# Performance work log

Hardware: AMD Instinct MI355X
Metric: run time of the kernel (lower is better)

## Reference

```python
import jax, jax.numpy as jnp
import numpy as np
import math

N, D = 4096, 1024


def setup_inputs() -> dict:
    key = jax.random.key(0)
    ks = jax.random.split(key, 8)
    vecs = jax.random.normal(ks[0], (N, D), dtype=jnp.float32)
    mass = jax.random.uniform(ks[1], (N,), dtype=jnp.float32)            # semantic mass in [0,1)
    hops = jax.random.uniform(ks[2], (N,), dtype=jnp.float32) * 5.0      # hop distances in [0,5)
    alive = jax.random.randint(ks[3], (N,), 0, 10) > 0
    is_photon = jax.random.randint(ks[4], (N,), 0, 10) == 0
    W_res_w = jax.random.normal(ks[5], (D, D), dtype=jnp.float32) / np.sqrt(D)
    W_res_b = jnp.zeros((D,), dtype=jnp.float32)
    w_conf_i = jax.random.normal(ks[6], (D,), dtype=jnp.float32) / np.sqrt(2 * D)
    w_conf_j = jax.random.normal(ks[7], (D,), dtype=jnp.float32) / np.sqrt(2 * D)
    b_conf = jnp.zeros((), dtype=jnp.float32)
    log_c = jnp.asarray(math.log(50.0), dtype=jnp.float32)  # 'relationship' domain
    log_G = jnp.zeros((), dtype=jnp.float32)
    return dict(vecs=vecs, mass=mass, hops=hops, alive=alive, is_photon=is_photon,
                W_res_w=W_res_w, W_res_b=W_res_b, w_conf_i=w_conf_i, w_conf_j=w_conf_j,
                b_conf=b_conf, log_c=log_c, log_G=log_G)


def reference(vecs, mass, hops, alive, is_photon, W_res_w, W_res_b,
              w_conf_i, w_conf_j, b_conf, log_c, log_G):
    n = vecs.shape[0]
    c = jnp.maximum(jnp.exp(log_c), 1e-6)
    G = jnp.exp(log_G)

    # Per-row quantities (phi() reads hops/photon from entity i).
    d_light = hops / c                                                   # [N]
    lam = jnp.where(is_photon, 1.0, jnp.exp(-d_light))                   # redshift, [N]
    r2 = jnp.maximum(d_light, 0.1) ** 2                                  # r_safe^2, [N]
    causal_decay = jnp.where(d_light <= 1.0, 1.0, jnp.exp(-d_light + 1.0))  # [N]

    # Causal mask: j must be strictly in the past (j < i).
    idx = jnp.arange(n)
    past = (idx[None, :] < idx[:, None]).astype(vecs.dtype)              # [N,N]
    C = past * causal_decay[:, None]

    # Gravity: G * m_i * m_j / r_i^2
    grav = G * (mass / r2)[:, None] * mass[None, :]                      # [N,N]

    # Resonance: cosine similarity of W_res projections (torch eps=1e-8 norm clamp).
    v = vecs @ W_res_w.T + W_res_b                                       # [N,D]
    vn = v / jnp.maximum(jnp.linalg.norm(v, axis=-1, keepdims=True), 1e-8)
    R = vn @ vn.T                                                        # [N,N]
    zero_norm = jnp.linalg.norm(vecs, axis=-1) < 1e-8                    # [N]
    R = jnp.where(zero_norm[:, None] | zero_norm[None, :], 0.0, R)

    # Conflict gate: sigmoid(W_conflict @ concat(v_i, v_j) + b) = sigmoid(s_i + s_j + b).
    s_i = vecs @ w_conf_i                                                # [N]
    s_j = vecs @ w_conf_j                                                # [N]
    conflict = jax.nn.sigmoid(s_i[:, None] + s_j[None, :] + b_conf)      # [N,N]

    phi_attract = lam[:, None] * grav * C * (0.5 + 0.5 * R)
    phi_repulse = -lam[:, None] * conflict * mass[:, None] * mass[None, :]
    phi = jnp.where(conflict > 0.8, phi_repulse, phi_attract)

    # Black holes and the diagonal produce zero field.
    gate = alive[:, None] & alive[None, :]
    phi = jnp.where(gate & (idx[:, None] != idx[None, :]), phi, 0.0)
    return phi
```

## Files before the change

kernel.cpp:

```cpp
#include <hip/hip_runtime.h>
#include <hip/hip_bf16.h>
#include <math.h>

#define NROW 4096
#define DIM  1024

typedef short v8s __attribute__((ext_vector_type(8)));
typedef float v4f __attribute__((ext_vector_type(4)));

#define GLD16(src, dst) __builtin_amdgcn_global_load_lds( \
    (const __attribute__((address_space(1))) void*)(src), \
    (__attribute__((address_space(3))) void*)(dst), 16, 0, 0)

__device__ __forceinline__ ushort f2bf(float f) {
    __hip_bfloat16 h = __float2bfloat16(f);
    union { __hip_bfloat16 h; ushort u; } x; x.h = h; return x.u;
}
__device__ __forceinline__ ushort4 cvt4(float4 a) {
    ushort4 r; r.x = f2bf(a.x); r.y = f2bf(a.y); r.z = f2bf(a.z); r.w = f2bf(a.w);
    return r;
}

__global__ __launch_bounds__(256) void k_stats(
    const float* vecs, const float* __restrict__ mass,
    const float* __restrict__ hops, const int* __restrict__ alive,
    const int* __restrict__ is_photon, const float* __restrict__ wci,
    const float* __restrict__ wcj, const float* __restrict__ logc,
    const float* __restrict__ logG, const float* __restrict__ bconf,
    const float* W,
    ushort* vsh, int vstr, ushort* wsh, int wstr,
    double* __restrict__ s_i, double* __restrict__ s_j,
    float* __restrict__ rowAtt, float* __restrict__ rowRep,
    float* __restrict__ massF, int* __restrict__ flags,
    float* __restrict__ rownorm)
{
    const int t = threadIdx.x;
    const int wid = t >> 6, lane = t & 63;

    if (blockIdx.x >= NROW / 4) {
        const int row = (blockIdx.x - NROW / 4) * 4 + wid;
        const float* wr = W + (size_t)row * DIM;
        ushort4 uc[4];
        #pragma unroll
        for (int q = 0; q < 4; ++q)
            uc[q] = cvt4(*(const float4*)&wr[lane * 4 + q * 256]);
        __syncthreads();
        ushort* wb = wsh + (size_t)row * wstr;
        #pragma unroll
        for (int q = 0; q < 4; ++q)
            *(ushort4*)&wb[lane * 4 + q * 256] = uc[q];
        return;
    }

    const int row = blockIdx.x * 4 + wid;
    const float* vr = vecs + (size_t)row * DIM;
    double di = 0.0, dj = 0.0, ss = 0.0;
    ushort4 uc[4];
    #pragma unroll
    for (int q = 0; q < 4; ++q) {
        int base = lane * 4 + q * 256;
        float4 pv = *(const float4*)&vr[base];
        float4 pi = *(const float4*)&wci[base];
        float4 pj = *(const float4*)&wcj[base];
        di += (double)pv.x * pi.x + (double)pv.y * pi.y + (double)pv.z * pi.z + (double)pv.w * pi.w;
        dj += (double)pv.x * pj.x + (double)pv.y * pj.y + (double)pv.z * pj.z + (double)pv.w * pj.w;
        ss += (double)pv.x * pv.x + (double)pv.y * pv.y + (double)pv.z * pv.z + (double)pv.w * pv.w;
        uc[q] = cvt4(pv);
    }
    __syncthreads();
    ushort* vb = vsh + (size_t)row * vstr;
    #pragma unroll
    for (int q = 0; q < 4; ++q)
        *(ushort4*)&vb[lane * 4 + q * 256] = uc[q];
    #pragma unroll
    for (int off = 32; off > 0; off >>= 1) {
        di += __shfl_down(di, off);
        dj += __shfl_down(dj, off);
        ss += __shfl_down(ss, off);
    }
    if (lane == 0) {
        double c  = fmax(exp((double)logc[0]), 1e-6);
        double G  = exp((double)logG[0]);
        double dl = (double)hops[row] / c;
        double lam = (is_photon[row] != 0) ? 1.0 : exp(-dl);
        double rs  = fmax(dl, 0.1);
        double cd  = (dl <= 1.0) ? 1.0 : exp(-dl + 1.0);
        double m   = (double)mass[row];
        s_i[row] = di;
        s_j[row] = dj + (double)bconf[0];
        rowAtt[row] = (float)(lam * G * m / (rs * rs) * cd);
        rowRep[row] = (float)(-lam * m);
        massF[row]  = (float)m;
        flags[row]  = ((alive[row] != 0) ? 1 : 0) | ((sqrt(ss) < 1e-8) ? 2 : 0);
        rownorm[row] = 0.0f;
    }
}

__global__ __launch_bounds__(256) void k_proj(
    const ushort* __restrict__ vsh, int vstr,
    const ushort* __restrict__ wsh, int wstr,
    const float* __restrict__ bias, ushort* __restrict__ vout,
    float* __restrict__ rownorm)
{
    __shared__ ushort As[64 * 64], Bs[64 * 64];
    const int t = threadIdx.x;
    const int m0 = blockIdx.y * 64, n0 = blockIdx.x * 64;
    const int wid = t >> 6, lane = t & 63;
    const int wm = wid >> 1, wn = wid & 1;
    const int quad = lane >> 4, l16 = lane & 15;
    const int sr = t >> 3, sc = t & 7;
    v4f acc[2][2];
    #pragma unroll
    for (int i = 0; i < 2; i++)
        #pragma unroll
        for (int j = 0; j < 2; j++) acc[i][j] = (v4f){0.f, 0.f, 0.f, 0.f};

    #pragma unroll
    for (int p = 0; p < 2; ++p) {
        int r = p * 32 + sr;
        int ksw = (sc ^ (r & 7)) * 8;
        GLD16(&vsh[(size_t)(m0 + r) * vstr + ksw], &As[p * 2048 + wid * 512]);
        GLD16(&wsh[(size_t)(n0 + r) * wstr + ksw], &Bs[p * 2048 + wid * 512]);
    }
    __syncthreads();

    for (int k0 = 0; k0 < DIM; k0 += 64) {
        #pragma unroll
        for (int ks = 0; ks < 2; ++ks) {
            v8s af[2], bfr[2];
            #pragma unroll
            for (int mi = 0; mi < 2; mi++) {
                int row = wm * 32 + mi * 16 + l16;
                af[mi] = *(const v8s*)&As[row * 64 + (((ks * 4 + quad) ^ (l16 & 7)) * 8)];
            }
            #pragma unroll
            for (int ni = 0; ni < 2; ni++) {
                int row = wn * 32 + ni * 16 + l16;
                bfr[ni] = *(const v8s*)&Bs[row * 64 + (((ks * 4 + quad) ^ (l16 & 7)) * 8)];
            }
            #pragma unroll
            for (int mi = 0; mi < 2; mi++)
                #pragma unroll
                for (int ni = 0; ni < 2; ni++)
                    acc[mi][ni] = __builtin_amdgcn_mfma_f32_16x16x32_bf16(af[mi], bfr[ni], acc[mi][ni], 0, 0, 0);
        }
        if (k0 + 64 < DIM) {
            __syncthreads();
            int k1 = k0 + 64;
            #pragma unroll
            for (int p = 0; p < 2; ++p) {
                int r = p * 32 + sr;
                int ksw = (sc ^ (r & 7)) * 8;
                GLD16(&vsh[(size_t)(m0 + r) * vstr + k1 + ksw], &As[p * 2048 + wid * 512]);
                GLD16(&wsh[(size_t)(n0 + r) * wstr + k1 + ksw], &Bs[p * 2048 + wid * 512]);
            }
            __syncthreads();
        }
    }

    float bcol[2];
    #pragma unroll
    for (int ni = 0; ni < 2; ni++) bcol[ni] = bias[n0 + wn * 32 + ni * 16 + l16];
    #pragma unroll
    for (int mi = 0; mi < 2; mi++)
        #pragma unroll
        for (int r = 0; r < 4; r++) {
            int row = m0 + wm * 32 + mi * 16 + quad * 4 + r;
            float ss = 0.0f;
            #pragma unroll
            for (int ni = 0; ni < 2; ni++) {
                int col = n0 + wn * 32 + ni * 16 + l16;
                float vv = acc[mi][ni][r] + bcol[ni];
                vout[(size_t)row * DIM + col] = f2bf(vv);
                ss += vv * vv;
            }
            #pragma unroll
            for (int off = 8; off > 0; off >>= 1) ss += __shfl_down(ss, off);
            if (l16 == 0) atomicAdd(&rownorm[row], ss);
        }
}

__global__ __launch_bounds__(256) void k_phi(
    const ushort* __restrict__ vn,
    const double* __restrict__ s_i, const double* __restrict__ s_j,
    const float* __restrict__ rowAtt, const float* __restrict__ rowRep,
    const float* __restrict__ massF, const int* __restrict__ flags,
    const float* __restrict__ rownorm, float* __restrict__ out)
{
    __shared__ ushort As[128 * 64], Bs[64 * 64];
    const int t = threadIdx.x;
    const int raw = blockIdx.x;
    const int id = (raw & 7) * 132 + (raw >> 3);
    int p = (int)((sqrtf(4.0f * (float)id + 1.0f) - 1.0f) * 0.5f);
    while ((p + 1) * (p + 2) <= id) ++p;
    while (p * (p + 1) > id) --p;
    const int j = id - p * (p + 1);
    const bool straddle = (j >= 2 * p);
    const int m0 = p * 128, n0 = j * 64;
    const int wid = t >> 6, lane = t & 63;
    const int wm = wid >> 1, wn = wid & 1;
    const int quad = lane >> 4, l16 = lane & 15;
    const int sr = t >> 3, sc = t & 7;
    const double LN4 = 1.3862943611198906;

    #pragma unroll
    for (int q = 0; q < 4; ++q) {
        int rr = q * 32 + sr;
        int ksw = (sc ^ (rr & 7)) * 8;
        GLD16(&vn[(size_t)(m0 + rr) * DIM + ksw], &As[q * 2048 + wid * 512]);
    }
    #pragma unroll
    for (int q = 0; q < 2; ++q) {
        int rr = q * 32 + sr;
        int ksw = (sc ^ (rr & 7)) * 8;
        GLD16(&vn[(size_t)(n0 + rr) * DIM + ksw], &Bs[q * 2048 + wid * 512]);
    }

    if (!straddle) {
        double csjL[4]; float cmL[4]; int colL[4];
        #pragma unroll
        for (int ni = 0; ni < 4; ni++) {
            int col = m0 + wn * 64 + ni * 16 + l16;
            colL[ni] = col;
            csjL[ni] = s_j[col];
            cmL[ni]  = (flags[col] & 1) ? massF[col] : 0.f;
        }
        #pragma unroll
        for (int mi = 0; mi < 2; mi++)
            #pragma unroll
            for (int rr = 0; rr < 4; rr++) {
                int row = n0 + wm * 32 + mi * 16 + quad * 4 + rr;
                double si = s_i[row];
                float  rRm = (flags[row] & 1) ? rowRep[row] : 0.f;
                size_t ob = (size_t)row * NROW;
                #pragma unroll
                for (int ni = 0; ni < 4; ni++) {
                    double x = si + csjL[ni];
                    float v = 0.f;
                    if (x > LN4) {
                        float e = __expf(-(float)x);
                        v = rRm * cmL[ni] * __builtin_amdgcn_rcpf(1.0f + e);
                    }
                    out[ob + colL[ni]] = v;
                }
            }
    }

    double csjH[2]; float cmn[2], cc[2]; int colH[2];
    #pragma unroll
    for (int ni = 0; ni < 2; ni++) {
        int col = n0 + wn * 32 + ni * 16 + l16;
        int cf = flags[col];
        float cma = (cf & 1) ? massF[col] : 0.f;
        colH[ni] = col;
        csjH[ni] = s_j[col];
        cmn[ni]  = cma;
        cc[ni]   = (cf & 2) ? 0.f
                 : cma * __builtin_amdgcn_rcpf(fmaxf(sqrtf(rownorm[col]), 1e-8f));
    }

    v4f acc[4][2];
    #pragma unroll
    for (int i = 0; i < 4; i++)
        #pragma unroll
        for (int jj = 0; jj < 2; jj++) acc[i][jj] = (v4f){0.f, 0.f, 0.f, 0.f};

    __syncthreads();
    for (int k0 = 0; k0 < DIM; k0 += 64) {
        #pragma unroll
        for (int ks = 0; ks < 2; ++ks) {
            v8s af[4], bfr[2];
            #pragma unroll
            for (int mi = 0; mi < 4; mi++) {
                int row = wm * 64 + mi * 16 + l16;
                af[mi] = *(const v8s*)&As[row * 64 + (((ks * 4 + quad) ^ (l16 & 7)) * 8)];
            }
            #pragma unroll
            for (int ni = 0; ni < 2; ni++) {
                int row = wn * 32 + ni * 16 + l16;
                bfr[ni] = *(const v8s*)&Bs[row * 64 + (((ks * 4 + quad) ^ (l16 & 7)) * 8)];
            }
            #pragma unroll
            for (int mi = 0; mi < 4; mi++)
                #pragma unroll
                for (int ni = 0; ni < 2; ni++)
                    acc[mi][ni] = __builtin_amdgcn_mfma_f32_16x16x32_bf16(af[mi], bfr[ni], acc[mi][ni], 0, 0, 0);
        }
        if (k0 + 64 < DIM) {
            __syncthreads();
            int k1 = k0 + 64;
            #pragma unroll
            for (int q = 0; q < 4; ++q) {
                int rr = q * 32 + sr;
                int ksw = (sc ^ (rr & 7)) * 8;
                GLD16(&vn[(size_t)(m0 + rr) * DIM + k1 + ksw], &As[q * 2048 + wid * 512]);
            }
            #pragma unroll
            for (int q = 0; q < 2; ++q) {
                int rr = q * 32 + sr;
                int ksw = (sc ^ (rr & 7)) * 8;
                GLD16(&vn[(size_t)(n0 + rr) * DIM + k1 + ksw], &Bs[q * 2048 + wid * 512]);
            }
            __syncthreads();
        }
    }

    #pragma unroll
    for (int mi = 0; mi < 4; mi++)
        #pragma unroll
        for (int rr = 0; rr < 4; rr++) {
            int row = m0 + wm * 64 + mi * 16 + quad * 4 + rr;
            int fi = flags[row];
            float rA  = rowAtt[row];
            float riv = __builtin_amdgcn_rcpf(fmaxf(sqrtf(rownorm[row]), 1e-8f));
            float a1  = (fi & 1) ? 0.5f * rA : 0.f;
            float a2  = ((fi & 3) == 1) ? 0.5f * rA * riv : 0.f;
            float rRm = (fi & 1) ? rowRep[row] : 0.f;
            double si = s_i[row];
            size_t ob = (size_t)row * NROW;
            #pragma unroll
            for (int ni = 0; ni < 2; ni++) {
                double x = si + csjH[ni];
                float  acv = acc[mi][ni][rr];
                float  att = fmaf(a2 * cc[ni], acv, a1 * cmn[ni]);
                float  e   = __expf(-(float)x);
                float  rep = rRm * cmn[ni] * __builtin_amdgcn_rcpf(1.0f + e);
                float  v   = (x > LN4) ? rep : att;
                if (straddle) {
                    int col = colH[ni];
                    if (col > row) v = (x > LN4) ? rep : 0.f;
                    if (col == row) v = 0.f;
                }
                out[ob + colH[ni]] = v;
            }
        }
}

extern "C" void kernel_launch(void* const* d_in, const int* in_sizes, int n_in,
                              void* d_out, int out_size, void* d_ws, size_t ws_size,
                              hipStream_t stream)
{
    const float* vecs      = (const float*)d_in[0];
    const float* mass      = (const float*)d_in[1];
    const float* hops      = (const float*)d_in[2];
    const int*   alive     = (const int*)d_in[3];
    const int*   is_photon = (const int*)d_in[4];
    const float* W         = (const float*)d_in[5];
    const float* Wb        = (const float*)d_in[6];
    const float* wci       = (const float*)d_in[7];
    const float* wcj       = (const float*)d_in[8];
    const float* bconf     = (const float*)d_in[9];
    const float* logc      = (const float*)d_in[10];
    const float* logG      = (const float*)d_in[11];

    char* ws = (char*)d_ws;
    double* s_i     = (double*)(ws);
    double* s_j     = (double*)(ws + 32768);
    float*  rowAtt  = (float*)(ws + 65536);
    float*  rowRep  = (float*)(ws + 81920);
    float*  massF   = (float*)(ws + 98304);
    int*    flagsA  = (int*)(ws + 114688);
    float*  rownorm = (float*)(ws + 131072);
    ushort* vn      = (ushort*)(ws + 147456);

    const size_t VSH_OFF = 147456 + (size_t)NROW * DIM * 2;
    const size_t WSH_OFF = VSH_OFF + (size_t)NROW * DIM * 2;
    const size_t NEED    = WSH_OFF + (size_t)DIM * DIM * 2;
    ushort *vsh, *wsh; int vstr, wstr;
    if (ws_size >= NEED) {
        vsh = (ushort*)(ws + VSH_OFF); vstr = DIM;
        wsh = (ushort*)(ws + WSH_OFF); wstr = DIM;
    } else {
        vsh = (ushort*)vecs + 1024; vstr = 2048;
        wsh = (ushort*)W + 1024;    wstr = 2048;
    }

    k_stats<<<dim3(NROW / 4 + DIM / 4), dim3(256), 0, stream>>>(
        vecs, mass, hops, alive, is_photon, wci, wcj, logc, logG, bconf, W,
        vsh, vstr, wsh, wstr,
        s_i, s_j, rowAtt, rowRep, massF, flagsA, rownorm);
    k_proj<<<dim3(DIM / 64, NROW / 64), dim3(256), 0, stream>>>(
        vsh, vstr, wsh, wstr, Wb, vn, rownorm);
    k_phi<<<dim3(1056), dim3(256), 0, stream>>>(
        vn, s_i, s_j, rowAtt, rowRep, massF, flagsA, rownorm, (float*)d_out);
}
```

Before: 175.1 us.

## Restructure phi kernel into single-wave 64x64 tiles with software-prefetched loads

The phi kernel moves from 256-thread blocks over a triangular 128x64 tiling to 4096 single-wavefront blocks over a full 64x64 grid. Upper-triangle tiles skip the GEMM and only write the repulsion term. Lower and diagonal tiles run a one-wave MFMA loop with explicit waitcnt, and the next k-tile's global-to-LDS loads are issued before the MFMAs instead of between barriers. This removes block-level syncs and the triangular index math, at the cost of less operand reuse per tile, more blocks, and a single LDS buffer whose refill must not overtake pending reads.

```diff
diff --git a/kernel.cpp b/kernel.cpp
--- a/kernel.cpp
+++ b/kernel.cpp
@@ -180,136 +180,110 @@
         }
 }
 
-__global__ __launch_bounds__(256) void k_phi(
+__global__ __launch_bounds__(64) void k_phi(
     const ushort* __restrict__ vn,
     const double* __restrict__ s_i, const double* __restrict__ s_j,
     const float* __restrict__ rowAtt, const float* __restrict__ rowRep,
     const float* __restrict__ massF, const int* __restrict__ flags,
     const float* __restrict__ rownorm, float* __restrict__ out)
 {
-    __shared__ ushort As[128 * 64], Bs[64 * 64];
-    const int t = threadIdx.x;
+    __shared__ ushort As[64 * 64], Bs[64 * 64];
     const int raw = blockIdx.x;
-    const int id = (raw & 7) * 132 + (raw >> 3);
-    int p = (int)((sqrtf(4.0f * (float)id + 1.0f) - 1.0f) * 0.5f);
-    while ((p + 1) * (p + 2) <= id) ++p;
-    while (p * (p + 1) > id) --p;
-    const int j = id - p * (p + 1);
-    const bool straddle = (j >= 2 * p);
-    const int m0 = p * 128, n0 = j * 64;
-    const int wid = t >> 6, lane = t & 63;
-    const int wm = wid >> 1, wn = wid & 1;
+    const int id = (raw & 7) * 512 + (raw >> 3);
+    const int bi = id >> 6, bj = id & 63;
+    const int m0 = bi * 64, n0 = bj * 64;
+    const int lane = threadIdx.x;
+    const double LN4 = 1.3862943611198906;
+
+    if (bj > bi) {
+        int col = n0 + lane;
+        double sj = s_j[col];
+        float  cm = (flags[col] & 1) ? massF[col] : 0.f;
+        #pragma unroll 4
+        for (int rr = 0; rr < 64; ++rr) {
+            int row = m0 + rr;
+            double x = s_i[row] + sj;
+            float rRm = (flags[row] & 1) ? rowRep[row] : 0.f;
+            float v = 0.f;
+            if (x > LN4) {
+                float e = __expf(-(float)x);
+                v = rRm * cm * __builtin_amdgcn_rcpf(1.0f + e);
+            }
+            out[(size_t)row * NROW + col] = v;
+        }
+        return;
+    }
+
+    const bool diag = (bi == bj);
     const int quad = lane >> 4, l16 = lane & 15;
-    const int sr = t >> 3, sc = t & 7;
-    const double LN4 = 1.3862943611198906;
-
-    #pragma unroll
-    for (int q = 0; q < 4; ++q) {
-        int rr = q * 32 + sr;
-        int ksw = (sc ^ (rr & 7)) * 8;
-        GLD16(&vn[(size_t)(m0 + rr) * DIM + ksw], &As[q * 2048 + wid * 512]);
-    }
-    #pragma unroll
-    for (int q = 0; q < 2; ++q) {
-        int rr = q * 32 + sr;
-        int ksw = (sc ^ (rr & 7)) * 8;
-        GLD16(&vn[(size_t)(n0 + rr) * DIM + ksw], &Bs[q * 2048 + wid * 512]);
-    }
-
-    if (!straddle) {
-        double csjL[4]; float cmL[4]; int colL[4];
-        #pragma unroll
-        for (int ni = 0; ni < 4; ni++) {
-            int col = m0 + wn * 64 + ni * 16 + l16;
-            colL[ni] = col;
-            csjL[ni] = s_j[col];
-            cmL[ni]  = (flags[col] & 1) ? massF[col] : 0.f;
-        }
-        #pragma unroll
-        for (int mi = 0; mi < 2; mi++)
-            #pragma unroll
-            for (int rr = 0; rr < 4; rr++) {
-                int row = n0 + wm * 32 + mi * 16 + quad * 4 + rr;
-                double si = s_i[row];
-                float  rRm = (flags[row] & 1) ? rowRep[row] : 0.f;
-                size_t ob = (size_t)row * NROW;
-                #pragma unroll
-                for (int ni = 0; ni < 4; ni++) {
-                    double x = si + csjL[ni];
-                    float v = 0.f;
-                    if (x > LN4) {
-                        float e = __expf(-(float)x);
-                        v = rRm * cmL[ni] * __builtin_amdgcn_rcpf(1.0f + e);
-                    }
-                    out[ob + colL[ni]] = v;
-                }
-            }
-    }
-
-    double csjH[2]; float cmn[2], cc[2]; int colH[2];
-    #pragma unroll
-    for (int ni = 0; ni < 2; ni++) {
-        int col = n0 + wn * 32 + ni * 16 + l16;
+    const int sr = lane >> 3, sc = lane & 7;
+
+    auto ISSUE = [&](int kt) {
+        const int k0 = kt * 64;
+        const int ksw = (sc ^ sr) * 8;
+        #pragma unroll
+        for (int q = 0; q < 8; ++q)
+            GLD16(&vn[(size_t)(m0 + q * 8 + sr) * DIM + k0 + ksw], &As[q * 512 + lane * 8]);
+        #pragma unroll
+        for (int q = 0; q < 8; ++q)
+            GLD16(&vn[(size_t)(n0 + q * 8 + sr) * DIM + k0 + ksw], &Bs[q * 512 + lane * 8]);
+    };
+
+    ISSUE(0);
+
+    double csjH[4]; float cmn[4], cc[4];
+    #pragma unroll
+    for (int ni = 0; ni < 4; ni++) {
+        int col = n0 + ni * 16 + l16;
         int cf = flags[col];
         float cma = (cf & 1) ? massF[col] : 0.f;
-        colH[ni] = col;
         csjH[ni] = s_j[col];
         cmn[ni]  = cma;
         cc[ni]   = (cf & 2) ? 0.f
                  : cma * __builtin_amdgcn_rcpf(fmaxf(sqrtf(rownorm[col]), 1e-8f));
     }
 
-    v4f acc[4][2];
+    v4f acc[4][4];
     #pragma unroll
     for (int i = 0; i < 4; i++)
         #pragma unroll
-        for (int jj = 0; jj < 2; jj++) acc[i][jj] = (v4f){0.f, 0.f, 0.f, 0.f};
-
-    __syncthreads();
-    for (int k0 = 0; k0 < DIM; k0 += 64) {
+        for (int j = 0; j < 4; j++) acc[i][j] = (v4f){0.f, 0.f, 0.f, 0.f};
+
+    for (int kt = 0; kt < 16; ++kt) {
+        asm volatile("s_waitcnt vmcnt(0)" ::: "memory");
+        __builtin_amdgcn_sched_barrier(0);
+        v8s af[2][4], bfr[2][4];
         #pragma unroll
         for (int ks = 0; ks < 2; ++ks) {
-            v8s af[4], bfr[2];
             #pragma unroll
             for (int mi = 0; mi < 4; mi++) {
-                int row = wm * 64 + mi * 16 + l16;
-                af[mi] = *(const v8s*)&As[row * 64 + (((ks * 4 + quad) ^ (l16 & 7)) * 8)];
-            }
-            #pragma unroll
-            for (int ni = 0; ni < 2; ni++) {
-                int row = wn * 32 + ni * 16 + l16;
-                bfr[ni] = *(const v8s*)&Bs[row * 64 + (((ks * 4 + quad) ^ (l16 & 7)) * 8)];
-            }
+                int row = mi * 16 + l16;
+                af[ks][mi] = *(const v8s*)&As[row * 64 + (((ks * 4 + quad) ^ (l16 & 7)) * 8)];
+            }
+            #pragma unroll
+            for (int ni = 0; ni < 4; ni++) {
+                int row = ni * 16 + l16;
+                bfr[ks][ni] = *(const v8s*)&Bs[row * 64 + (((ks * 4 + quad) ^ (l16 & 7)) * 8)];
+            }
+        }
+        asm volatile("s_waitcnt lgkmcnt(0)" ::: "memory");
+        __builtin_amdgcn_sched_barrier(0);
+        if (kt + 1 < 16) ISSUE(kt + 1);
+        #pragma unroll
+        for (int ks = 0; ks < 2; ++ks)
             #pragma unroll
             for (int mi = 0; mi < 4; mi++)
                 #pragma unroll
-                for (int ni = 0; ni < 2; ni++)
-                    acc[mi][ni] = __builtin_amdgcn_mfma_f32_16x16x32_bf16(af[mi], bfr[ni], acc[mi][ni], 0, 0, 0);
-        }
-        if (k0 + 64 < DIM) {
-            __syncthreads();
-            int k1 = k0 + 64;
-            #pragma unroll
-            for (int q = 0; q < 4; ++q) {
-                int rr = q * 32 + sr;
-                int ksw = (sc ^ (rr & 7)) * 8;
-                GLD16(&vn[(size_t)(m0 + rr) * DIM + k1 + ksw], &As[q * 2048 + wid * 512]);
-            }
-            #pragma unroll
-            for (int q = 0; q < 2; ++q) {
-                int rr = q * 32 + sr;
-                int ksw = (sc ^ (rr & 7)) * 8;
-                GLD16(&vn[(size_t)(n0 + rr) * DIM + k1 + ksw], &Bs[q * 2048 + wid * 512]);
-            }
-            __syncthreads();
-        }
+                for (int ni = 0; ni < 4; ni++)
+                    acc[mi][ni] = __builtin_amdgcn_mfma_f32_16x16x32_bf16(
+                        af[ks][mi], bfr[ks][ni], acc[mi][ni], 0, 0, 0);
     }
 
     #pragma unroll
     for (int mi = 0; mi < 4; mi++)
         #pragma unroll
         for (int rr = 0; rr < 4; rr++) {
-            int row = m0 + wm * 64 + mi * 16 + quad * 4 + rr;
+            int row = m0 + mi * 16 + quad * 4 + rr;
             int fi = flags[row];
             float rA  = rowAtt[row];
             float riv = __builtin_amdgcn_rcpf(fmaxf(sqrtf(rownorm[row]), 1e-8f));
@@ -319,19 +293,19 @@
             double si = s_i[row];
             size_t ob = (size_t)row * NROW;
             #pragma unroll
-            for (int ni = 0; ni < 2; ni++) {
+            for (int ni = 0; ni < 4; ni++) {
+                int col = n0 + ni * 16 + l16;
                 double x = si + csjH[ni];
                 float  acv = acc[mi][ni][rr];
                 float  att = fmaf(a2 * cc[ni], acv, a1 * cmn[ni]);
                 float  e   = __expf(-(float)x);
                 float  rep = rRm * cmn[ni] * __builtin_amdgcn_rcpf(1.0f + e);
                 float  v   = (x > LN4) ? rep : att;
-                if (straddle) {
-                    int col = colH[ni];
+                if (diag) {
                     if (col > row) v = (x > LN4) ? rep : 0.f;
                     if (col == row) v = 0.f;
                 }
-                out[ob + colH[ni]] = v;
+                out[ob + col] = v;
             }
         }
 }
@@ -381,6 +355,6 @@
         s_i, s_j, rowAtt, rowRep, massF, flagsA, rownorm);
     k_proj<<<dim3(DIM / 64, NROW / 64), dim3(256), 0, stream>>>(
         vsh, vstr, wsh, wstr, Wb, vn, rownorm);
-    k_phi<<<dim3(1056), dim3(256), 0, stream>>>(
+    k_phi<<<dim3(4096), dim3(64), 0, stream>>>(
         vn, s_i, s_j, rowAtt, rowRep, massF, flagsA, rownorm, (float*)d_out);
 }
```

After: 180.9 us. 1.03x slower.

## Use square 64x64 triangular tiles with 128-thread blocks in phi kernel

Applied to the files above, without the earlier changes.

Replaces the 128x64 rectangular tiling over the lower triangle with 64x64 square tiles: 2080 blocks of two waves each, one per lower-triangular tile, with each block also writing the mirrored upper tile's repulse-only values. This cuts wasted MFMA work on the diagonal-straddling tiles and yields more, smaller blocks for better load balance. In exchange it gives less operand reuse per loaded byte and more total global traffic for the vn tiles.

```diff
diff --git a/kernel.cpp b/kernel.cpp
--- a/kernel.cpp
+++ b/kernel.cpp
@@ -180,47 +180,41 @@
         }
 }
 
-__global__ __launch_bounds__(256) void k_phi(
+__global__ __launch_bounds__(128) void k_phi(
     const ushort* __restrict__ vn,
     const double* __restrict__ s_i, const double* __restrict__ s_j,
     const float* __restrict__ rowAtt, const float* __restrict__ rowRep,
     const float* __restrict__ massF, const int* __restrict__ flags,
     const float* __restrict__ rownorm, float* __restrict__ out)
 {
-    __shared__ ushort As[128 * 64], Bs[64 * 64];
+    __shared__ ushort As[64 * 64], Bs[64 * 64];
     const int t = threadIdx.x;
     const int raw = blockIdx.x;
-    const int id = (raw & 7) * 132 + (raw >> 3);
-    int p = (int)((sqrtf(4.0f * (float)id + 1.0f) - 1.0f) * 0.5f);
-    while ((p + 1) * (p + 2) <= id) ++p;
-    while (p * (p + 1) > id) --p;
-    const int j = id - p * (p + 1);
-    const bool straddle = (j >= 2 * p);
-    const int m0 = p * 128, n0 = j * 64;
+    const int id = (raw & 7) * 260 + (raw >> 3);
+    int r = (int)((sqrtf(8.0f * (float)id + 1.0f) - 1.0f) * 0.5f);
+    while ((((r + 1) * (r + 2)) >> 1) <= id) ++r;
+    while (((r * (r + 1)) >> 1) > id) --r;
+    const int bi = r, bj = id - ((r * (r + 1)) >> 1);
+    const bool diag = (bi == bj);
+    const int m0 = bi * 64, n0 = bj * 64;
     const int wid = t >> 6, lane = t & 63;
-    const int wm = wid >> 1, wn = wid & 1;
     const int quad = lane >> 4, l16 = lane & 15;
     const int sr = t >> 3, sc = t & 7;
     const double LN4 = 1.3862943611198906;
 
     #pragma unroll
     for (int q = 0; q < 4; ++q) {
-        int rr = q * 32 + sr;
+        int rr = q * 16 + sr;
         int ksw = (sc ^ (rr & 7)) * 8;
-        GLD16(&vn[(size_t)(m0 + rr) * DIM + ksw], &As[q * 2048 + wid * 512]);
-    }
-    #pragma unroll
-    for (int q = 0; q < 2; ++q) {
-        int rr = q * 32 + sr;
-        int ksw = (sc ^ (rr & 7)) * 8;
-        GLD16(&vn[(size_t)(n0 + rr) * DIM + ksw], &Bs[q * 2048 + wid * 512]);
-    }
-
-    if (!straddle) {
+        GLD16(&vn[(size_t)(m0 + rr) * DIM + ksw], &As[q * 1024 + wid * 512]);
+        GLD16(&vn[(size_t)(n0 + rr) * DIM + ksw], &Bs[q * 1024 + wid * 512]);
+    }
+
+    if (!diag) {
         double csjL[4]; float cmL[4]; int colL[4];
         #pragma unroll
         for (int ni = 0; ni < 4; ni++) {
-            int col = m0 + wn * 64 + ni * 16 + l16;
+            int col = m0 + ni * 16 + l16;
             colL[ni] = col;
             csjL[ni] = s_j[col];
             cmL[ni]  = (flags[col] & 1) ? massF[col] : 0.f;
@@ -229,7 +223,7 @@
         for (int mi = 0; mi < 2; mi++)
             #pragma unroll
             for (int rr = 0; rr < 4; rr++) {
-                int row = n0 + wm * 32 + mi * 16 + quad * 4 + rr;
+                int row = n0 + wid * 32 + mi * 16 + quad * 4 + rr;
                 double si = s_i[row];
                 float  rRm = (flags[row] & 1) ? rowRep[row] : 0.f;
                 size_t ob = (size_t)row * NROW;
@@ -246,44 +240,43 @@
             }
     }
 
-    double csjH[2]; float cmn[2], cc[2]; int colH[2];
-    #pragma unroll
-    for (int ni = 0; ni < 2; ni++) {
-        int col = n0 + wn * 32 + ni * 16 + l16;
+    double csjH[4]; float cmn[4], cc[4];
+    #pragma unroll
+    for (int ni = 0; ni < 4; ni++) {
+        int col = n0 + ni * 16 + l16;
         int cf = flags[col];
         float cma = (cf & 1) ? massF[col] : 0.f;
-        colH[ni] = col;
         csjH[ni] = s_j[col];
         cmn[ni]  = cma;
         cc[ni]   = (cf & 2) ? 0.f
                  : cma * __builtin_amdgcn_rcpf(fmaxf(sqrtf(rownorm[col]), 1e-8f));
     }
 
-    v4f acc[4][2];
-    #pragma unroll
-    for (int i = 0; i < 4; i++)
-        #pragma unroll
-        for (int jj = 0; jj < 2; jj++) acc[i][jj] = (v4f){0.f, 0.f, 0.f, 0.f};
+    v4f acc[2][4];
+    #pragma unroll
+    for (int i = 0; i < 2; i++)
+        #pragma unroll
+        for (int j = 0; j < 4; j++) acc[i][j] = (v4f){0.f, 0.f, 0.f, 0.f};
 
     __syncthreads();
     for (int k0 = 0; k0 < DIM; k0 += 64) {
         #pragma unroll
         for (int ks = 0; ks < 2; ++ks) {
-            v8s af[4], bfr[2];
-            #pragma unroll
-            for (int mi = 0; mi < 4; mi++) {
-                int row = wm * 64 + mi * 16 + l16;
+            v8s af[2], bfr[4];
+            #pragma unroll
+            for (int mi = 0; mi < 2; mi++) {
+                int row = wid * 32 + mi * 16 + l16;
                 af[mi] = *(const v8s*)&As[row * 64 + (((ks * 4 + quad) ^ (l16 & 7)) * 8)];
             }
             #pragma unroll
-            for (int ni = 0; ni < 2; ni++) {
-                int row = wn * 32 + ni * 16 + l16;
+            for (int ni = 0; ni < 4; ni++) {
+                int row = ni * 16 + l16;
                 bfr[ni] = *(const v8s*)&Bs[row * 64 + (((ks * 4 + quad) ^ (l16 & 7)) * 8)];
             }
             #pragma unroll
-            for (int mi = 0; mi < 4; mi++)
+            for (int mi = 0; mi < 2; mi++)
                 #pragma unroll
-                for (int ni = 0; ni < 2; ni++)
+                for (int ni = 0; ni < 4; ni++)
                     acc[mi][ni] = __builtin_amdgcn_mfma_f32_16x16x32_bf16(af[mi], bfr[ni], acc[mi][ni], 0, 0, 0);
         }
         if (k0 + 64 < DIM) {
@@ -291,25 +284,20 @@
             int k1 = k0 + 64;
             #pragma unroll
             for (int q = 0; q < 4; ++q) {
-                int rr = q * 32 + sr;
+                int rr = q * 16 + sr;
                 int ksw = (sc ^ (rr & 7)) * 8;
-                GLD16(&vn[(size_t)(m0 + rr) * DIM + k1 + ksw], &As[q * 2048 + wid * 512]);
-            }
-            #pragma unroll
-            for (int q = 0; q < 2; ++q) {
-                int rr = q * 32 + sr;
-                int ksw = (sc ^ (rr & 7)) * 8;
-                GLD16(&vn[(size_t)(n0 + rr) * DIM + k1 + ksw], &Bs[q * 2048 + wid * 512]);
+                GLD16(&vn[(size_t)(m0 + rr) * DIM + k1 + ksw], &As[q * 1024 + wid * 512]);
+                GLD16(&vn[(size_t)(n0 + rr) * DIM + k1 + ksw], &Bs[q * 1024 + wid * 512]);
             }
             __syncthreads();
         }
     }
 
     #pragma unroll
-    for (int mi = 0; mi < 4; mi++)
+    for (int mi = 0; mi < 2; mi++)
         #pragma unroll
         for (int rr = 0; rr < 4; rr++) {
-            int row = m0 + wm * 64 + mi * 16 + quad * 4 + rr;
+            int row = m0 + wid * 32 + mi * 16 + quad * 4 + rr;
             int fi = flags[row];
             float rA  = rowAtt[row];
             float riv = __builtin_amdgcn_rcpf(fmaxf(sqrtf(rownorm[row]), 1e-8f));
@@ -319,19 +307,19 @@
             double si = s_i[row];
             size_t ob = (size_t)row * NROW;
             #pragma unroll
-            for (int ni = 0; ni < 2; ni++) {
+            for (int ni = 0; ni < 4; ni++) {
+                int col = n0 + ni * 16 + l16;
                 double x = si + csjH[ni];
                 float  acv = acc[mi][ni][rr];
                 float  att = fmaf(a2 * cc[ni], acv, a1 * cmn[ni]);
                 float  e   = __expf(-(float)x);
                 float  rep = rRm * cmn[ni] * __builtin_amdgcn_rcpf(1.0f + e);
                 float  v   = (x > LN4) ? rep : att;
-                if (straddle) {
-                    int col = colH[ni];
+                if (diag) {
                     if (col > row) v = (x > LN4) ? rep : 0.f;
                     if (col == row) v = 0.f;
                 }
-                out[ob + colH[ni]] = v;
+                out[ob + col] = v;
             }
         }
 }
@@ -381,6 +369,6 @@
         s_i, s_j, rowAtt, rowRep, massF, flagsA, rownorm);
     k_proj<<<dim3(DIM / 64, NROW / 64), dim3(256), 0, stream>>>(
         vsh, vstr, wsh, wstr, Wb, vn, rownorm);
-    k_phi<<<dim3(1056), dim3(256), 0, stream>>>(
+    k_phi<<<dim3(2080), dim3(128), 0, stream>>>(
         vn, s_i, s_j, rowAtt, rowRep, massF, flagsA, rownorm, (float*)d_out);
 }
```

Measured after the change: 168.5 us. 1.04x faster.
